# Kernel tuning notes

Hardware: AMD Instinct MI355X
Metric: run time of the kernel (lower is better)

## Reference

```python
import jax, jax.numpy as jnp
import numpy as np

N = 128 * 1562          # total nodes (128 graphs x 1562 nodes)
E = 3_200_000           # edges (avg degree ~16)
B = 128                 # number of graphs
FEAT = 64               # config.feature_dim
DIMS = (32, 32, 32, 1)  # config.gcnn_dims
TOTAL_DIM = sum(DIMS)   # 97
K = 60                  # config.top_k
NUM_CLASSES = 9


def setup_inputs() -> dict:
    key = jax.random.key(0)
    ks = jax.random.split(key, 16)
    row = jax.random.randint(ks[0], (E,), 0, N)
    col = jax.random.randint(ks[1], (E,), 0, N)
    values = jnp.ones((E,), jnp.float32)
    # degree-inverse diagonal (original passes it as a sparse diag matrix)
    deg = jax.ops.segment_sum(values, row, num_segments=N)
    deg_inv = 1.0 / (deg + 1.0)
    features = jax.random.uniform(ks[2], (N, FEAT), jnp.float32, 0.0, 257.0)
    npg = N // B
    starts = jnp.arange(B, dtype=jnp.int64) * npg
    graph_indexes = jnp.stack([starts, starts + npg], axis=1)
    # GCN weight matrices (truncated normal in original)
    in_dim = FEAT
    Ws = []
    for i, d in enumerate(DIMS):
        Ws.append(jax.random.normal(ks[3 + i], (in_dim, d), jnp.float32) * 0.1)
        in_dim = d
    conv1_w = jax.random.normal(ks[8], (TOTAL_DIM, 1, 16), jnp.float32) * 0.05
    conv1_b = jnp.zeros((16,), jnp.float32)
    conv2_w = jax.random.normal(ks[9], (4, 16, 32), jnp.float32) * 0.1
    conv2_b = jnp.zeros((32,), jnp.float32)
    dense_w = jax.random.normal(ks[10], (30 * 32, 16), jnp.float32) * 0.05
    dense_b = jnp.zeros((16,), jnp.float32)
    out_w = jax.random.normal(ks[11], (16, NUM_CLASSES), jnp.float32) * 0.1
    out_b = jnp.zeros((NUM_CLASSES,), jnp.float32)
    return {
        "row": row, "col": col, "values": values, "deg_inv": deg_inv,
        "features": features, "graph_indexes": graph_indexes,
        "W0": Ws[0], "W1": Ws[1], "W2": Ws[2], "W3": Ws[3],
        "conv1_w": conv1_w, "conv1_b": conv1_b,
        "conv2_w": conv2_w, "conv2_b": conv2_b,
        "dense_w": dense_w, "dense_b": dense_b,
        "out_w": out_w, "out_b": out_b,
    }


def _forward(row, col, values, deg_inv, features, graph_indexes,
             Ws, conv1_w, conv1_b, conv2_w, conv2_b,
             dense_w, dense_b, out_w, out_b):
    n = features.shape[0]
    # Rescaling(1/257)
    Z = features / 257.0
    # stacked GCN layers: tanh(D^-1 (A Z + Z) W)
    outs = []
    for W in Ws:
        AZ = jax.ops.segment_sum(values[:, None] * Z[col], row, num_segments=n) + Z
        Z = jnp.tanh(deg_inv[:, None] * (AZ @ W))
        outs.append(Z)
    G = jnp.concatenate(outs, axis=1)  # [N, TOTAL_DIM]
    D = G.shape[1]
    b = graph_indexes.shape[0]
    starts = graph_indexes[:, 0]
    # per-node graph id (spans are contiguous and ascending)
    gid = jnp.searchsorted(starts, jnp.arange(n), side="right") - 1
    # segmented top-k by last GCN channel: stable sort by (graph, -last_col)
    order = jnp.lexsort((-G[:, -1], gid))
    sg = gid[order]
    rank = jnp.arange(n) - starts[sg]
    rc = jnp.where(rank < K, rank, K)  # overflow rows land in a dummy slot
    pooled = jnp.zeros((b, K + 1, D), G.dtype).at[sg, rc].set(G[order])[:, :K, :]
    # 1D CNN readout
    x = pooled.reshape(b, K * D, 1)
    dn = ("NWC", "WIO", "NWC")
    y = jax.nn.relu(jax.lax.conv_general_dilated(x, conv1_w, (D,), "SAME", dimension_numbers=dn) + conv1_b)
    y = jax.lax.reduce_window(y, -jnp.inf, jax.lax.max, (1, 2, 1), (1, 2, 1), "VALID")
    y = jax.nn.relu(jax.lax.conv_general_dilated(y, conv2_w, (1,), "SAME", dimension_numbers=dn) + conv2_b)
    y = y.reshape(b, -1)
    h = jax.nn.relu(y @ dense_w + dense_b)
    # dropout is identity at inference (training=False)
    return h @ out_w + out_b


def reference(row, col, values, deg_inv, features, graph_indexes,
              W0, W1, W2, W3, conv1_w, conv1_b, conv2_w, conv2_b,
              dense_w, dense_b, out_w, out_b):
    return _forward(row, col, values, deg_inv, features, graph_indexes,
                    [W0, W1, W2, W3], conv1_w, conv1_b, conv2_w, conv2_b,
                    dense_w, dense_b, out_w, out_b)
```

## Files before the change

kernel.cpp:

```cpp
#include <hip/hip_runtime.h>
#include <math.h>

static __device__ __forceinline__ float tanhf_cr(float x) {
  return (float)tanh((double)x);
}

#define TIE_BAND 4.5e-7f
#define DGATE    1.9e-3

__global__ void k_zdiv(const float* __restrict__ f, float* __restrict__ z, int n) {
  int stride = gridDim.x * blockDim.x;
  for (int i = blockIdx.x * blockDim.x + threadIdx.x; i < n; i += stride)
    z[i] = __fdiv_rn(f[i], 257.0f);
}

static __device__ __forceinline__ int deg_from_inv(float di) {
  return (int)rintf(__fdiv_rn(1.0f, di)) - 1;
}

__global__ void k_scanpart(const float* __restrict__ deg_inv, int* __restrict__ bsum,
                           int N, int chunk) {
  __shared__ int red[256];
  int b = blockIdx.x;
  int s = b * chunk, e = s + chunk;
  if (e > N) e = N;
  int sum = 0;
  for (int i = s + threadIdx.x; i < e; i += 256) sum += deg_from_inv(deg_inv[i]);
  red[threadIdx.x] = sum;
  __syncthreads();
  for (int off = 128; off; off >>= 1) {
    if (threadIdx.x < off) red[threadIdx.x] += red[threadIdx.x + off];
    __syncthreads();
  }
  if (threadIdx.x == 0) bsum[b] = red[0];
}

__global__ void k_scanmid(int* __restrict__ bsum) {
  __shared__ int sh[1024];
  int t = threadIdx.x;
  sh[t] = bsum[t];
  __syncthreads();
  for (int off = 1; off < 1024; off <<= 1) {
    int v = (t >= off) ? sh[t - off] : 0;
    __syncthreads();
    sh[t] += v;
    __syncthreads();
  }
  bsum[t] = (t == 0) ? 0 : sh[t - 1];
}

__global__ void k_scanout(const float* __restrict__ deg_inv, const int* __restrict__ bsum,
                          int* __restrict__ rs, int N, int chunk, int E) {
  __shared__ int sh[256];
  int b = blockIdx.x;
  int s = b * chunk, e = s + chunk;
  if (e > N) e = N;
  int t = threadIdx.x;
  int idx = s + t;
  int v = (idx < e) ? deg_from_inv(deg_inv[idx]) : 0;
  sh[t] = v;
  __syncthreads();
  for (int off = 1; off < 256; off <<= 1) {
    int u = (t >= off) ? sh[t - off] : 0;
    __syncthreads();
    sh[t] += u;
    __syncthreads();
  }
  if (idx < e) rs[idx] = bsum[b] + sh[t] - v;
  if (b == 0 && t == 0) rs[N] = E;
}

__global__ void k_scatter(const int* __restrict__ row, const int* __restrict__ col,
                          const int* __restrict__ rs, int* __restrict__ cnt2,
                          unsigned long long* __restrict__ packed, int E) {
  int stride = gridDim.x * blockDim.x;
  for (int i = blockIdx.x * blockDim.x + threadIdx.x; i < E; i += stride) {
    int r = row[i];
    int p = rs[r] + atomicAdd(&cnt2[r], 1);
    packed[p] = ((unsigned long long)(unsigned)i << 32) | (unsigned)col[i];
  }
}

__global__ void k_rowsortw(const int* __restrict__ rs, unsigned long long* __restrict__ packed,
                           int* __restrict__ ccol, int N) {
  int wid = threadIdx.x >> 6;
  int lane = threadIdx.x & 63;
  int node = blockIdx.x * 4 + wid;
  if (node >= N) return;
  int s = rs[node], e = rs[node + 1];
  int deg = e - s;
  if (deg <= 1) {
    if (deg == 1 && lane == 0) ccol[s] = (int)(packed[s] & 0xFFFFFFFFull);
    return;
  }
  if (deg <= 64) {
    unsigned long long v = (lane < deg) ? packed[s + lane] : ~0ULL;
#pragma unroll
    for (int k = 2; k <= 64; k <<= 1) {
#pragma unroll
      for (int j = k >> 1; j; j >>= 1) {
        unsigned long long o = __shfl_xor(v, j, 64);
        bool up = ((lane & k) == 0);
        bool keepmin = (((lane & j) == 0) == up);
        bool take = keepmin ? (o < v) : (o > v);
        if (take) v = o;
      }
    }
    if (lane < deg) ccol[s + lane] = (int)(v & 0xFFFFFFFFull);
  } else if (lane == 0) {
    for (int a = s + 1; a < e; ++a) {
      unsigned long long key = packed[a];
      int b = a - 1;
      while (b >= s && packed[b] > key) { packed[b + 1] = packed[b]; --b; }
      packed[b + 1] = key;
    }
    for (int p = s; p < e; ++p) ccol[p] = (int)(packed[p] & 0xFFFFFFFFull);
  }
}

template <int DIN, int DOUT>
__global__ void k_layer(const float* __restrict__ Zin, float* __restrict__ Zout,
                        const int* __restrict__ rs, const int* __restrict__ ccol,
                        const float* __restrict__ deg_inv,
                        const float* __restrict__ W, int N) {
  constexpr int NPB = 256 / DIN;
  __shared__ float sW[DIN * DOUT];
  __shared__ float az[NPB][DIN];
  for (int i = threadIdx.x; i < DIN * DOUT; i += 256) sW[i] = W[i];
  __syncthreads();
  int ln = threadIdx.x / DIN;
  int f = threadIdx.x % DIN;
  int ntiles = (N + NPB - 1) / NPB;
  for (int tile = blockIdx.x; tile < ntiles; tile += gridDim.x) {
    int node = tile * NPB + ln;
    if (node < N) {
      int s = rs[node], e = rs[node + 1];
      if (DIN == 64) {
        s = __builtin_amdgcn_readfirstlane(s);
        e = __builtin_amdgcn_readfirstlane(e);
      }
      float acc = 0.0f;
      int p = s;
      for (; p + 8 <= e; p += 8) {
        int c0 = ccol[p], c1 = ccol[p + 1], c2 = ccol[p + 2], c3 = ccol[p + 3];
        int c4 = ccol[p + 4], c5 = ccol[p + 5], c6 = ccol[p + 6], c7 = ccol[p + 7];
        float v0 = Zin[(size_t)c0 * DIN + f], v1 = Zin[(size_t)c1 * DIN + f];
        float v2 = Zin[(size_t)c2 * DIN + f], v3 = Zin[(size_t)c3 * DIN + f];
        float v4 = Zin[(size_t)c4 * DIN + f], v5 = Zin[(size_t)c5 * DIN + f];
        float v6 = Zin[(size_t)c6 * DIN + f], v7 = Zin[(size_t)c7 * DIN + f];
        acc = __fadd_rn(acc, v0); acc = __fadd_rn(acc, v1);
        acc = __fadd_rn(acc, v2); acc = __fadd_rn(acc, v3);
        acc = __fadd_rn(acc, v4); acc = __fadd_rn(acc, v5);
        acc = __fadd_rn(acc, v6); acc = __fadd_rn(acc, v7);
      }
      for (; p + 4 <= e; p += 4) {
        int c0 = ccol[p], c1 = ccol[p + 1], c2 = ccol[p + 2], c3 = ccol[p + 3];
        float v0 = Zin[(size_t)c0 * DIN + f], v1 = Zin[(size_t)c1 * DIN + f];
        float v2 = Zin[(size_t)c2 * DIN + f], v3 = Zin[(size_t)c3 * DIN + f];
        acc = __fadd_rn(acc, v0); acc = __fadd_rn(acc, v1);
        acc = __fadd_rn(acc, v2); acc = __fadd_rn(acc, v3);
      }
      for (; p < e; ++p) acc = __fadd_rn(acc, Zin[(size_t)ccol[p] * DIN + f]);
      acc = __fadd_rn(acc, Zin[(size_t)node * DIN + f]);
      az[ln][f] = acc;
    }
    __syncthreads();
    int t = threadIdx.x;
    if (t < NPB * DOUT) {
      int ln2 = t / DOUT, c2 = t % DOUT;
      int node2 = tile * NPB + ln2;
      if (node2 < N) {
        float d = 0.0f;
#pragma unroll
        for (int k = 0; k < DIN; ++k)
          d = __fmaf_rn(az[ln2][k], sW[k * DOUT + c2], d);
        d = __fmul_rn(deg_inv[node2], d);
        Zout[(size_t)node2 * DOUT + c2] = tanhf_cr(d);
      }
    }
    __syncthreads();
  }
}

__global__ void k_sorttop(const float* __restrict__ Z4, int* __restrict__ topidx,
                          int* __restrict__ pairrank, int npg) {
  __shared__ unsigned long long keys[2048];
  __shared__ float vals[61];
  int g = blockIdx.x;
  int base = g * npg;
  for (int i = threadIdx.x; i < 2048; i += blockDim.x) {
    unsigned long long kk = ~0ULL;
    if (i < npg) {
      unsigned u = __float_as_uint(Z4[base + i]);
      if ((u & 0x7FFFFFFFu) == 0u) u = 0u;
      unsigned m = (u & 0x80000000u) ? ~u : (u | 0x80000000u);
      unsigned a = ~m;
      kk = ((unsigned long long)a << 32) | (unsigned)i;
    }
    keys[i] = kk;
  }
  __syncthreads();
  for (int k = 2; k <= 2048; k <<= 1) {
    for (int j = k >> 1; j > 0; j >>= 1) {
      for (int i = threadIdx.x; i < 2048; i += blockDim.x) {
        int ixj = i ^ j;
        if (ixj > i) {
          unsigned long long a = keys[i], b = keys[ixj];
          bool asc = ((i & k) == 0);
          if (asc ? (a > b) : (a < b)) { keys[i] = b; keys[ixj] = a; }
        }
      }
      __syncthreads();
    }
  }
  int tid = threadIdx.x;
  if (tid < 61) {
    topidx[g * 61 + tid] = base + (int)(keys[tid] & 0xFFFFFFFFu);
    unsigned a = (unsigned)(keys[tid] >> 32);
    unsigned m = ~a;
    unsigned u = (m & 0x80000000u) ? (m & 0x7FFFFFFFu) : ~m;
    vals[tid] = __uint_as_float(u);
  }
  __syncthreads();
  if (tid == 0) {
    int best = -1;
    float bestd = 0.0f;
    for (int r = 1; r < 60; r += 2) {
      float dv = __fsub_rn(vals[r], vals[r + 1]);
      if (dv <= TIE_BAND && (best == -1 || dv < bestd)) { best = r; bestd = dv; }
    }
    pairrank[g] = best;
  }
}

__global__ void k_cnn2(const float* __restrict__ Z1, const float* __restrict__ Z2,
                       const float* __restrict__ Z3, const float* __restrict__ Z4,
                       const int* __restrict__ topidx, const int* __restrict__ pairrank,
                       const float* __restrict__ w1, const float* __restrict__ b1,
                       const float* __restrict__ w2, const float* __restrict__ b2,
                       const float* __restrict__ wd, const float* __restrict__ bd,
                       const float* __restrict__ wo, const float* __restrict__ bo,
                       float* __restrict__ out) {
  __shared__ float sx[61 * 97];
  __shared__ double y1[60 * 16];
  __shared__ double y2[30 * 16];
  __shared__ double y3[30 * 32];
  __shared__ double h[16];
  __shared__ double lg[2][9];
  __shared__ int perm[61];
  __shared__ int avgflag;
  int g = blockIdx.x;
  int tid = threadIdx.x;
  for (int t = tid; t < 61 * 97; t += blockDim.x) {
    int r = t / 97, d = t - r * 97;
    int node = topidx[g * 61 + r];
    float v;
    if (d < 32)      v = Z1[(size_t)node * 32 + d];
    else if (d < 64) v = Z2[(size_t)node * 32 + (d - 32)];
    else if (d < 96) v = Z3[(size_t)node * 32 + (d - 64)];
    else             v = Z4[node];
    sx[t] = v;
  }
  int pr = pairrank[g];
  int nvar = (pr >= 0) ? 2 : 1;
  __syncthreads();
  for (int var = 0; var < nvar; ++var) {
    if (tid < 61) {
      int p = tid;
      if (var == 1) { if (tid == pr) p = pr + 1; else if (tid == pr + 1) p = pr; }
      perm[tid] = p;
    }
    __syncthreads();
    for (int t = tid; t < 60 * 16; t += blockDim.x) {
      int p = t >> 4, c = t & 15;
      const float* rowp = &sx[perm[p] * 97];
      double a = 0.0;
      for (int k = 0; k < 97; ++k) a = fma((double)rowp[k], (double)w1[k * 16 + c], a);
      a += (double)b1[c];
      y1[t] = a > 0.0 ? a : 0.0;
    }
    __syncthreads();
    for (int t = tid; t < 30 * 16; t += blockDim.x) {
      int p = t >> 4, c = t & 15;
      double a = y1[(2 * p) * 16 + c], b = y1[(2 * p + 1) * 16 + c];
      y2[t] = a > b ? a : b;
    }
    __syncthreads();
    for (int t = tid; t < 30 * 32; t += blockDim.x) {
      int p = t >> 5, c = t & 31;
      double a = 0.0;
      for (int dw = 0; dw < 4; ++dw) {
        int pp = p + dw - 1;
        if (pp < 0 || pp >= 30) continue;
        for (int ci = 0; ci < 16; ++ci)
          a = fma(y2[pp * 16 + ci], (double)w2[(dw * 16 + ci) * 32 + c], a);
      }
      a += (double)b2[c];
      y3[t] = a > 0.0 ? a : 0.0;
    }
    __syncthreads();
    for (int t = tid; t < 16; t += blockDim.x) {
      double a = 0.0;
      for (int k = 0; k < 960; ++k) a = fma(y3[k], (double)wd[k * 16 + t], a);
      a += (double)bd[t];
      h[t] = a > 0.0 ? a : 0.0;
    }
    __syncthreads();
    if (tid < 9) {
      double a = 0.0;
      for (int k = 0; k < 16; ++k) a = fma(h[k], (double)wo[k * 9 + tid], a);
      a += (double)bo[tid];
      lg[var][tid] = a;
    }
    __syncthreads();
  }
  if (tid == 0) {
    int f = 0;
    if (nvar == 2) {
      double md = 0.0;
      for (int k = 0; k < 9; ++k) {
        double d = lg[1][k] - lg[0][k];
        if (d < 0) d = -d;
        if (d > md) md = d;
      }
      f = (md <= DGATE) ? 1 : 0;
    }
    avgflag = f;
  }
  __syncthreads();
  if (tid < 9) {
    double v = avgflag ? 0.5 * (lg[0][tid] + lg[1][tid]) : lg[0][tid];
    out[g * 9 + tid] = (float)v;
  }
}

extern "C" void kernel_launch(void* const* d_in, const int* in_sizes, int n_in,
                              void* d_out, int out_size, void* d_ws, size_t ws_size,
                              hipStream_t stream) {
  (void)n_in; (void)ws_size;
  const int* row = (const int*)d_in[0];
  const int* col = (const int*)d_in[1];
  const float* deg_inv = (const float*)d_in[3];
  const float* features = (const float*)d_in[4];
  const float* W0 = (const float*)d_in[6];
  const float* W1 = (const float*)d_in[7];
  const float* W2 = (const float*)d_in[8];
  const float* W3 = (const float*)d_in[9];
  const float* c1w = (const float*)d_in[10];
  const float* c1b = (const float*)d_in[11];
  const float* c2w = (const float*)d_in[12];
  const float* c2b = (const float*)d_in[13];
  const float* dnw = (const float*)d_in[14];
  const float* dnb = (const float*)d_in[15];
  const float* ow = (const float*)d_in[16];
  const float* ob = (const float*)d_in[17];

  const int E = in_sizes[0];
  const int N = in_sizes[4] / 64;
  const int B = out_size / 9;
  const int npg = N / B;

  char* wp = (char*)d_ws;
  auto alloc = [&](size_t bytes) -> char* {
    char* r = wp;
    wp += (bytes + 255) & ~(size_t)255;
    return r;
  };
  float* Z0 = (float*)alloc((size_t)N * 64 * 4);
  float* Z1 = (float*)alloc((size_t)N * 32 * 4);
  float* Z2 = (float*)alloc((size_t)N * 32 * 4);
  float* Z3 = (float*)alloc((size_t)N * 32 * 4);
  float* Z4 = (float*)alloc((size_t)N * 4);
  int* cnt2 = (int*)alloc((size_t)N * 4);
  int* rs = (int*)alloc((size_t)(N + 1) * 4);
  unsigned long long* packed = (unsigned long long*)alloc((size_t)E * 8);
  int* ccol = (int*)alloc((size_t)E * 4);
  int* bsum = (int*)alloc((size_t)1024 * 4);
  int* topidx = (int*)alloc((size_t)B * 61 * 4);
  int* pairrank = (int*)alloc((size_t)B * 4);

  const int chunk = (N + 1023) / 1024;

  hipMemsetAsync(cnt2, 0, (size_t)N * 4, stream);
  k_zdiv<<<2048, 256, 0, stream>>>(features, Z0, N * 64);
  k_scanpart<<<1024, 256, 0, stream>>>(deg_inv, bsum, N, chunk);
  k_scanmid<<<1, 1024, 0, stream>>>(bsum);
  k_scanout<<<1024, 256, 0, stream>>>(deg_inv, bsum, rs, N, chunk, E);
  k_scatter<<<2048, 256, 0, stream>>>(row, col, rs, cnt2, packed, E);
  k_rowsortw<<<(N + 3) / 4, 256, 0, stream>>>(rs, packed, ccol, N);

  {
    int ntiles = (N + 3) / 4;
    int g = ntiles < 8192 ? ntiles : 8192;
    k_layer<64, 32><<<g, 256, 0, stream>>>(Z0, Z1, rs, ccol, deg_inv, W0, N);
  }
  {
    int ntiles = (N + 7) / 8;
    int g = ntiles < 8192 ? ntiles : 8192;
    k_layer<32, 32><<<g, 256, 0, stream>>>(Z1, Z2, rs, ccol, deg_inv, W1, N);
    k_layer<32, 32><<<g, 256, 0, stream>>>(Z2, Z3, rs, ccol, deg_inv, W2, N);
    k_layer<32, 1><<<g, 256, 0, stream>>>(Z3, Z4, rs, ccol, deg_inv, W3, N);
  }
  k_sorttop<<<B, 256, 0, stream>>>(Z4, topidx, pairrank, npg);
  k_cnn2<<<B, 256, 0, stream>>>(Z1, Z2, Z3, Z4, topidx, pairrank,
                                c1w, c1b, c2w, c2b, dnw, dnb, ow, ob, (float*)d_out);
}
```

Baseline: 879.5 us.

## Band edge scatter by row range per XCD and deepen gather unroll to 16

The edge scatter now runs 8 passes over the row array. In each pass, blocks assigned to a given XCD (blockIdx & 7) only handle edges whose row falls in one of 64 row bands. The intent is to keep each XCD's atomics and packed writes inside a narrow address range so they stay in that XCD's L2, at the cost of reading row[] eight times. The layer gather loop also gains a 16-wide batch that issues all index loads, then all feature loads, before accumulating, to raise memory-level parallelism.

```diff
diff --git a/kernel.cpp b/kernel.cpp
--- a/kernel.cpp
+++ b/kernel.cpp
@@ -70,14 +70,25 @@
   if (b == 0 && t == 0) rs[N] = E;
 }
 
-__global__ void k_scatter(const int* __restrict__ row, const int* __restrict__ col,
-                          const int* __restrict__ rs, int* __restrict__ cnt2,
-                          unsigned long long* __restrict__ packed, int E) {
-  int stride = gridDim.x * blockDim.x;
-  for (int i = blockIdx.x * blockDim.x + threadIdx.x; i < E; i += stride) {
-    int r = row[i];
-    int p = rs[r] + atomicAdd(&cnt2[r], 1);
-    packed[p] = ((unsigned long long)(unsigned)i << 32) | (unsigned)col[i];
+__global__ void k_scatterb(const int* __restrict__ row, const int* __restrict__ col,
+                           const int* __restrict__ rs, int* __restrict__ cnt2,
+                           unsigned long long* __restrict__ packed, int E, int subband) {
+  int xcd = blockIdx.x & 7;
+  int rank = blockIdx.x >> 3;
+  int nblk = gridDim.x >> 3;
+  int stride = nblk * blockDim.x;
+  int i0 = rank * blockDim.x + threadIdx.x;
+  for (int pass = 0; pass < 8; ++pass) {
+    int lo = (pass * 8 + xcd) * subband;
+    int hi = lo + subband;
+#pragma unroll 4
+    for (int i = i0; i < E; i += stride) {
+      int r = row[i];
+      if (r >= lo && r < hi) {
+        int p = rs[r] + atomicAdd(&cnt2[r], 1);
+        packed[p] = ((unsigned long long)(unsigned)i << 32) | (unsigned)col[i];
+      }
+    }
   }
 }
 
@@ -118,6 +129,21 @@
   }
 }
 
+template <int DIN, int UN>
+static __device__ __forceinline__ float edge_batch(const float* __restrict__ Zin,
+                                                   const int* __restrict__ ccol,
+                                                   int p, int f, float acc) {
+  int c[UN];
+  float v[UN];
+#pragma unroll
+  for (int u = 0; u < UN; ++u) c[u] = ccol[p + u];
+#pragma unroll
+  for (int u = 0; u < UN; ++u) v[u] = Zin[(size_t)c[u] * DIN + f];
+#pragma unroll
+  for (int u = 0; u < UN; ++u) acc = __fadd_rn(acc, v[u]);
+  return acc;
+}
+
 template <int DIN, int DOUT>
 __global__ void k_layer(const float* __restrict__ Zin, float* __restrict__ Zout,
                         const int* __restrict__ rs, const int* __restrict__ ccol,
@@ -141,25 +167,9 @@
       }
       float acc = 0.0f;
       int p = s;
-      for (; p + 8 <= e; p += 8) {
-        int c0 = ccol[p], c1 = ccol[p + 1], c2 = ccol[p + 2], c3 = ccol[p + 3];
-        int c4 = ccol[p + 4], c5 = ccol[p + 5], c6 = ccol[p + 6], c7 = ccol[p + 7];
-        float v0 = Zin[(size_t)c0 * DIN + f], v1 = Zin[(size_t)c1 * DIN + f];
-        float v2 = Zin[(size_t)c2 * DIN + f], v3 = Zin[(size_t)c3 * DIN + f];
-        float v4 = Zin[(size_t)c4 * DIN + f], v5 = Zin[(size_t)c5 * DIN + f];
-        float v6 = Zin[(size_t)c6 * DIN + f], v7 = Zin[(size_t)c7 * DIN + f];
-        acc = __fadd_rn(acc, v0); acc = __fadd_rn(acc, v1);
-        acc = __fadd_rn(acc, v2); acc = __fadd_rn(acc, v3);
-        acc = __fadd_rn(acc, v4); acc = __fadd_rn(acc, v5);
-        acc = __fadd_rn(acc, v6); acc = __fadd_rn(acc, v7);
-      }
-      for (; p + 4 <= e; p += 4) {
-        int c0 = ccol[p], c1 = ccol[p + 1], c2 = ccol[p + 2], c3 = ccol[p + 3];
-        float v0 = Zin[(size_t)c0 * DIN + f], v1 = Zin[(size_t)c1 * DIN + f];
-        float v2 = Zin[(size_t)c2 * DIN + f], v3 = Zin[(size_t)c3 * DIN + f];
-        acc = __fadd_rn(acc, v0); acc = __fadd_rn(acc, v1);
-        acc = __fadd_rn(acc, v2); acc = __fadd_rn(acc, v3);
-      }
+      for (; p + 16 <= e; p += 16) acc = edge_batch<DIN, 16>(Zin, ccol, p, f, acc);
+      for (; p + 8 <= e; p += 8)   acc = edge_batch<DIN, 8>(Zin, ccol, p, f, acc);
+      for (; p + 4 <= e; p += 4)   acc = edge_batch<DIN, 4>(Zin, ccol, p, f, acc);
       for (; p < e; ++p) acc = __fadd_rn(acc, Zin[(size_t)ccol[p] * DIN + f]);
       acc = __fadd_rn(acc, Zin[(size_t)node * DIN + f]);
       az[ln][f] = acc;
@@ -380,13 +390,14 @@
   int* pairrank = (int*)alloc((size_t)B * 4);
 
   const int chunk = (N + 1023) / 1024;
+  const int subband = (N + 63) / 64;
 
   hipMemsetAsync(cnt2, 0, (size_t)N * 4, stream);
   k_zdiv<<<2048, 256, 0, stream>>>(features, Z0, N * 64);
   k_scanpart<<<1024, 256, 0, stream>>>(deg_inv, bsum, N, chunk);
   k_scanmid<<<1, 1024, 0, stream>>>(bsum);
   k_scanout<<<1024, 256, 0, stream>>>(deg_inv, bsum, rs, N, chunk, E);
-  k_scatter<<<2048, 256, 0, stream>>>(row, col, rs, cnt2, packed, E);
+  k_scatterb<<<4096, 256, 0, stream>>>(row, col, rs, cnt2, packed, E, subband);
   k_rowsortw<<<(N + 3) / 4, 256, 0, stream>>>(rs, packed, ccol, N);
 
   {
```

Measured after the change: 1.005 ms. 1.14x slower.
